# Optimization experiments

Hardware: AMD Instinct MI355X
Metric: run time of the kernel (lower is better)

## Reference

```python
import jax, jax.numpy as jnp
import numpy as np

T, B, NA = 32, 32, 5          # timesteps, envs, actions
HID, FEAT = 256, 512          # lstm hidden, cnn features
IN_DIM = FEAT + NA            # lstm input size (517)
FLAT = 64 * 7 * 7             # cnn flatten size (3136)


def _conv(x, w, b, s):
    # x: NCHW, w: OIHW, VALID padding, stride s
    y = jax.lax.conv_general_dilated(x, w, (s, s), 'VALID',
                                     dimension_numbers=('NCHW', 'OIHW', 'NCHW'))
    return y + b[None, :, None, None]


def setup_inputs() -> dict:
    key = jax.random.key(0)
    ks = jax.random.split(key, 24)
    p = lambda k, shape: (jax.random.normal(k, shape, jnp.float32) * 0.05)
    return {
        'image': jax.random.uniform(ks[0], (T * B, 3, 84, 84), jnp.float32) * 255.0,
        'last_action': jax.random.randint(ks[1], (T * B,), 0, NA),
        'done': jax.random.bernoulli(ks[2], 0.05, (T * B,)).astype(jnp.float32),
        'h0': jnp.zeros((B, HID), jnp.float32),
        'c0': jnp.zeros((B, HID), jnp.float32),
        # NatureCNN params
        'W1': p(ks[3], (32, 3, 8, 8)), 'b1': jnp.zeros((32,), jnp.float32),
        'W2': p(ks[4], (64, 32, 4, 4)), 'b2': jnp.zeros((64,), jnp.float32),
        'W3': p(ks[5], (64, 64, 3, 3)), 'b3': jnp.zeros((64,), jnp.float32),
        'Wfc': p(ks[6], (FEAT, FLAT)), 'bfc': jnp.zeros((FEAT,), jnp.float32),
        # LSTM params (torch gate order i,f,g,o)
        'W_ih': p(ks[7], (4 * HID, IN_DIM)), 'W_hh': p(ks[8], (4 * HID, HID)),
        'b_ih': jnp.zeros((4 * HID,), jnp.float32), 'b_hh': jnp.zeros((4 * HID,), jnp.float32),
        # policy MLP (hidden 64, tanh)
        'Wp1': p(ks[9], (64, HID)), 'bp1': jnp.zeros((64,), jnp.float32),
        'Wp2': p(ks[10], (NA, 64)) * 0.01, 'bp2': jnp.zeros((NA,), jnp.float32),
        # value MLP
        'Wv1': p(ks[11], (64, HID)), 'bv1': jnp.zeros((64,), jnp.float32),
        'Wv2': p(ks[12], (1, 64)), 'bv2': jnp.zeros((1,), jnp.float32),
    }


def reference(image, last_action, done, h0, c0,
              W1, b1, W2, b2, W3, b3, Wfc, bfc,
              W_ih, W_hh, b_ih, b_hh,
              Wp1, bp1, Wp2, bp2, Wv1, bv1, Wv2, bv2):
    # --- extract: NatureCNN + one-hot(last_action) ---
    x = image / 255.0
    x = jax.nn.relu(_conv(x, W1, b1, 4))   # (TB,32,20,20)
    x = jax.nn.relu(_conv(x, W2, b2, 2))   # (TB,64,9,9)
    x = jax.nn.relu(_conv(x, W3, b3, 1))   # (TB,64,7,7)
    x = x.reshape(x.shape[0], -1)
    feat = jax.nn.relu(x @ Wfc.T + bfc)    # (TB,512)
    oh = jax.nn.one_hot(last_action, NA, dtype=feat.dtype)
    xs = jnp.concatenate([feat, oh], axis=1).reshape(T, B, IN_DIM)
    ds = done.reshape(T, B)

    # --- remember: done-masked LSTM recurrence (torch gate order i,f,g,o) ---
    def step(carry, inp):
        h, c = carry
        xt, dt = inp
        m = (1.0 - dt)[:, None]
        h = h * m
        c = c * m
        g = xt @ W_ih.T + b_ih + h @ W_hh.T + b_hh   # (B, 4*HID)
        i, f, gg, o = jnp.split(g, 4, axis=1)
        c = jax.nn.sigmoid(f) * c + jax.nn.sigmoid(i) * jnp.tanh(gg)
        h = jax.nn.sigmoid(o) * jnp.tanh(c)
        return (h, c), h

    (hT, cT), hs = jax.lax.scan(step, (h0, c0), (xs, ds))
    h = hs.reshape(T * B, HID)

    # --- heads ---
    logits = jnp.tanh(h @ Wp1.T + bp1) @ Wp2.T + bp2   # (TB, NA)
    v = jnp.tanh(h @ Wv1.T + bv1) @ Wv2.T + bv2        # (TB, 1)
    return logits, v, hT, cT
```

## Files before the change

### kernel.cpp

```cpp
#include <hip/hip_runtime.h>
#include <math.h>

typedef float  f4v __attribute__((ext_vector_type(4)));
typedef short  s8v __attribute__((ext_vector_type(8)));
typedef int    i4v __attribute__((ext_vector_type(4)));

__device__ __forceinline__ float sigm(float x) { return 1.f / (1.f + expf(-x)); }
__device__ __forceinline__ unsigned short f2bf(float f) {
    unsigned int u = __float_as_uint(f);
    return (unsigned short)((u + 0x7FFF + ((u >> 16) & 1)) >> 16);
}
__device__ __forceinline__ s8v pack8(float4 a, float4 b) {
    union { unsigned short u[8]; s8v v; } r;
    r.u[0] = f2bf(a.x); r.u[1] = f2bf(a.y); r.u[2] = f2bf(a.z); r.u[3] = f2bf(a.w);
    r.u[4] = f2bf(b.x); r.u[5] = f2bf(b.y); r.u[6] = f2bf(b.z); r.u[7] = f2bf(b.w);
    return r.v;
}

__global__ __launch_bounds__(256) void k_amax(const float* __restrict__ Whh,
                                              unsigned int* __restrict__ amax_bits) {
    int i = blockIdx.x * 256 + threadIdx.x;
    float v = fabsf(Whh[i]);
#pragma unroll
    for (int o = 1; o < 64; o <<= 1) v = fmaxf(v, __shfl_xor(v, o));
    if ((threadIdx.x & 63) == 0) atomicMax(amax_bits, __float_as_uint(v));
}

__global__ __launch_bounds__(256) void k_prep(const float* __restrict__ W2, const float* __restrict__ W3,
                                              const float* __restrict__ Wfc, const float* __restrict__ Wih,
                                              const float* __restrict__ W1, const float* __restrict__ Whh,
                                              const unsigned int* __restrict__ amax_bits,
                                              unsigned short* __restrict__ W2p, unsigned short* __restrict__ W3p,
                                              unsigned short* __restrict__ Wfcp, unsigned short* __restrict__ Wihp,
                                              unsigned short* __restrict__ W1p, signed char* __restrict__ Wq) {
    int i = blockIdx.x * 256 + threadIdx.x;
    if (i < 32768) {
        W2p[i] = f2bf(W2[i]);
    } else if (i < 98304) {
        int j = i - 32768;
        int co = j >> 10, r = j & 1023, ci = r >> 4, s = r & 15, ky = s >> 2, kx = s & 3;
        W3p[j] = (ky < 3 && kx < 3) ? f2bf(W3[((co * 64 + ci) * 3 + ky) * 3 + kx]) : (unsigned short)0;
    } else if (i < 1703936) {
        int j = i - 98304;
        Wfcp[j] = f2bf(Wfc[j]);
    } else if (i < 2228224) {
        int j = i - 1703936;
        int n = j >> 9, k = j & 511;
        Wihp[j] = f2bf(Wih[n * 517 + k]);
    } else if (i < 2234368) {
        int j = i - 2228224;
        W1p[j] = f2bf(W1[j] * (1.f / 255.f));
    } else if (i < 2496512) {
        int j = i - 2234368;
        float amax = __uint_as_float(amax_bits[0]);
        float s = 127.f / amax;
        int qv = (int)rintf(Whh[j] * s);
        qv = qv > 127 ? 127 : (qv < -127 ? -127 : qv);
        Wq[j] = (signed char)qv;
    }
}

__global__ __launch_bounds__(256) void k_conv1(const float* __restrict__ img,
                                               const unsigned short* __restrict__ Bw,
                                               const float* __restrict__ bias,
                                               unsigned short* __restrict__ out) {
    __shared__ unsigned short c1s[32][260];
    int lane = threadIdx.x & 63, w = threadIdx.x >> 6;
    int l15 = lane & 15, q = lane >> 4;
    int m0 = blockIdx.x * 256;
    const float* Ap[4];
#pragma unroll
    for (int mf = 0; mf < 4; ++mf) {
        int m = m0 + w * 64 + mf * 16 + l15;
        int im = m / 400, p = m - im * 400;
        int oy = p / 20, ox = p - oy * 20;
        Ap[mf] = img + im * 21168 + oy * 336 + ox * 4;
    }
    const unsigned short* Bp0 = Bw + l15 * 192 + q * 8;
    const unsigned short* Bp1 = Bw + (16 + l15) * 192 + q * 8;
    s8v bf0[6], bf1[6];
#pragma unroll
    for (int ks = 0; ks < 6; ++ks) {
        bf0[ks] = *(const s8v*)(Bp0 + ks * 32);
        bf1[ks] = *(const s8v*)(Bp1 + ks * 32);
    }
    f4v acc[8];
#pragma unroll
    for (int i = 0; i < 8; ++i) acc[i] = (f4v){0.f, 0.f, 0.f, 0.f};
#pragma unroll
    for (int ks = 0; ks < 6; ++ks) {
        int k0 = ks * 32 + q * 8;
        int c = k0 >> 6, ky = (k0 >> 3) & 7;
        int roff = c * 7056 + ky * 84;
        s8v ua[4];
#pragma unroll
        for (int mf = 0; mf < 4; ++mf) {
            float4 a0 = *(const float4*)(Ap[mf] + roff);
            float4 a1 = *(const float4*)(Ap[mf] + roff + 4);
            ua[mf] = pack8(a0, a1);
        }
#pragma unroll
        for (int mf = 0; mf < 4; ++mf) {
            acc[mf * 2 + 0] = __builtin_amdgcn_mfma_f32_16x16x32_bf16(ua[mf], bf0[ks], acc[mf * 2 + 0], 0, 0, 0);
            acc[mf * 2 + 1] = __builtin_amdgcn_mfma_f32_16x16x32_bf16(ua[mf], bf1[ks], acc[mf * 2 + 1], 0, 0, 0);
        }
    }
#pragma unroll
    for (int nf = 0; nf < 2; ++nf) {
        int n = nf * 16 + l15;
        float b = bias[n];
#pragma unroll
        for (int mf = 0; mf < 4; ++mf) {
#pragma unroll
            for (int r = 0; r < 4; ++r) {
                int ml = w * 64 + mf * 16 + q * 4 + r;
                float v = acc[mf * 2 + nf][r] + b;
                c1s[n][ml] = f2bf(v > 0.f ? v : 0.f);
            }
        }
    }
    __syncthreads();
#pragma unroll
    for (int seg = 0; seg < 32; ++seg) {
        int flat = seg * 256 + threadIdx.x;
        int n = flat >> 8, ml = flat & 255;
        int m = m0 + ml;
        int im = m / 400, p = m - im * 400;
        out[(im * 32 + n) * 400 + p] = c1s[n][ml];
    }
}

__global__ __launch_bounds__(256) void k_conv2(const unsigned short* __restrict__ A,
                                               const unsigned short* __restrict__ Bw,
                                               const float* __restrict__ bias,
                                               unsigned short* __restrict__ out) {
    __shared__ unsigned short c2s[64][136];
    int lane = threadIdx.x & 63, w = threadIdx.x >> 6;
    int l15 = lane & 15, q = lane >> 4;
    int m0 = blockIdx.x * 128;
    int ma = m0 + w * 32 + l15, mb = ma + 16;
    int ia = ma / 81, pa = ma - ia * 81; int oya = pa / 9, oxa = pa - oya * 9;
    int ib = mb / 81, pb = mb - ib * 81; int oyb = pb / 9, oxb = pb - oyb * 9;
    const unsigned short* Aa = A + ia * 12800 + oya * 40 + oxa * 2 + (q & 1) * 40;
    const unsigned short* Ab = A + ib * 12800 + oyb * 40 + oxb * 2 + (q & 1) * 40;
    int ci0 = q >> 1;
    const unsigned short* B0 = Bw + (l15) * 512 + q * 8;
    const unsigned short* B1 = Bw + (16 + l15) * 512 + q * 8;
    const unsigned short* B2 = Bw + (32 + l15) * 512 + q * 8;
    const unsigned short* B3 = Bw + (48 + l15) * 512 + q * 8;
    f4v acc[8];
#pragma unroll
    for (int i = 0; i < 8; ++i) acc[i] = (f4v){0.f, 0.f, 0.f, 0.f};
    for (int c = 0; c < 16; ++c) {
        int ci = 2 * c + ci0;
        const unsigned short* pa_ = Aa + ci * 400;
        const unsigned short* pb_ = Ab + ci * 400;
        union { unsigned int u[4]; s8v v; } ua, ub;
        ua.u[0] = *(const unsigned int*)(pa_);      ua.u[1] = *(const unsigned int*)(pa_ + 2);
        ua.u[2] = *(const unsigned int*)(pa_ + 20); ua.u[3] = *(const unsigned int*)(pa_ + 22);
        ub.u[0] = *(const unsigned int*)(pb_);      ub.u[1] = *(const unsigned int*)(pb_ + 2);
        ub.u[2] = *(const unsigned int*)(pb_ + 20); ub.u[3] = *(const unsigned int*)(pb_ + 22);
        s8v b0 = *(const s8v*)B0, b1 = *(const s8v*)B1, b2 = *(const s8v*)B2, b3 = *(const s8v*)B3;
        B0 += 32; B1 += 32; B2 += 32; B3 += 32;
        acc[0] = __builtin_amdgcn_mfma_f32_16x16x32_bf16(ua.v, b0, acc[0], 0, 0, 0);
        acc[1] = __builtin_amdgcn_mfma_f32_16x16x32_bf16(ua.v, b1, acc[1], 0, 0, 0);
        acc[2] = __builtin_amdgcn_mfma_f32_16x16x32_bf16(ua.v, b2, acc[2], 0, 0, 0);
        acc[3] = __builtin_amdgcn_mfma_f32_16x16x32_bf16(ua.v, b3, acc[3], 0, 0, 0);
        acc[4] = __builtin_amdgcn_mfma_f32_16x16x32_bf16(ub.v, b0, acc[4], 0, 0, 0);
        acc[5] = __builtin_amdgcn_mfma_f32_16x16x32_bf16(ub.v, b1, acc[5], 0, 0, 0);
        acc[6] = __builtin_amdgcn_mfma_f32_16x16x32_bf16(ub.v, b2, acc[6], 0, 0, 0);
        acc[7] = __builtin_amdgcn_mfma_f32_16x16x32_bf16(ub.v, b3, acc[7], 0, 0, 0);
    }
#pragma unroll
    for (int nf = 0; nf < 4; ++nf) {
        int n = nf * 16 + l15;
        float b = bias[n];
#pragma unroll
        for (int mf = 0; mf < 2; ++mf) {
#pragma unroll
            for (int r = 0; r < 4; ++r) {
                int ml = w * 32 + mf * 16 + q * 4 + r;
                float v = acc[mf * 4 + nf][r] + b;
                c2s[n][ml] = f2bf(v > 0.f ? v : 0.f);
            }
        }
    }
    __syncthreads();
#pragma unroll
    for (int seg = 0; seg < 32; ++seg) {
        int flat = seg * 256 + threadIdx.x;
        int n = flat >> 7, ml = flat & 127;
        int m = m0 + ml;
        int im = m / 81, p = m - im * 81;
        out[im * 5184 + n * 81 + p] = c2s[n][ml];
    }
}

__global__ __launch_bounds__(256) void k_conv3(const unsigned short* __restrict__ A,
                                               const unsigned short* __restrict__ Bw,
                                               const float* __restrict__ bias,
                                               unsigned short* __restrict__ out) {
    __shared__ unsigned short c3s[64][136];
    int lane = threadIdx.x & 63, w = threadIdx.x >> 6;
    int l15 = lane & 15, q = lane >> 4;
    int m0 = blockIdx.x * 128;
    int ma = m0 + w * 32 + l15, mb = ma + 16;
    int ia = ma / 49, pa = ma - ia * 49; int oya = pa / 7, oxa = pa - oya * 7;
    int ib = mb / 49, pb = mb - ib * 49; int oyb = pb / 7, oxb = pb - oyb * 7;
    int ky0 = (q & 1) * 2;
    int r0off = ky0 * 9;
    int r1off = (ky0 + 1 > 2 ? 2 : ky0 + 1) * 9;
    int zr = q & 1;
    const unsigned short* Aa = A + ia * 5184 + oya * 9 + oxa;
    const unsigned short* Ab = A + ib * 5184 + oyb * 9 + oxb;
    int ci0 = q >> 1;
    const unsigned short* B0 = Bw + (l15) * 1024 + q * 8;
    const unsigned short* B1 = Bw + (16 + l15) * 1024 + q * 8;
    const unsigned short* B2 = Bw + (32 + l15) * 1024 + q * 8;
    const unsigned short* B3 = Bw + (48 + l15) * 1024 + q * 8;
    f4v acc[8];
#pragma unroll
    for (int i = 0; i < 8; ++i) acc[i] = (f4v){0.f, 0.f, 0.f, 0.f};
    for (int c = 0; c < 32; ++c) {
        int ci = 2 * c + ci0;
        const unsigned short* pa_ = Aa + ci * 81;
        const unsigned short* pb_ = Ab + ci * 81;
        s8v av, bv;
        av[0] = pa_[r0off]; av[1] = pa_[r0off + 1]; av[2] = pa_[r0off + 2]; av[3] = 0;
        av[4] = zr ? (short)0 : (short)pa_[r1off];
        av[5] = zr ? (short)0 : (short)pa_[r1off + 1];
        av[6] = zr ? (short)0 : (short)pa_[r1off + 2];
        av[7] = 0;
        bv[0] = pb_[r0off]; bv[1] = pb_[r0off + 1]; bv[2] = pb_[r0off + 2]; bv[3] = 0;
        bv[4] = zr ? (short)0 : (short)pb_[r1off];
        bv[5] = zr ? (short)0 : (short)pb_[r1off + 1];
        bv[6] = zr ? (short)0 : (short)pb_[r1off + 2];
        bv[7] = 0;
        s8v b0 = *(const s8v*)B0, b1 = *(const s8v*)B1, b2 = *(const s8v*)B2, b3 = *(const s8v*)B3;
        B0 += 32; B1 += 32; B2 += 32; B3 += 32;
        acc[0] = __builtin_amdgcn_mfma_f32_16x16x32_bf16(av, b0, acc[0], 0, 0, 0);
        acc[1] = __builtin_amdgcn_mfma_f32_16x16x32_bf16(av, b1, acc[1], 0, 0, 0);
        acc[2] = __builtin_amdgcn_mfma_f32_16x16x32_bf16(av, b2, acc[2], 0, 0, 0);
        acc[3] = __builtin_amdgcn_mfma_f32_16x16x32_bf16(av, b3, acc[3], 0, 0, 0);
        acc[4] = __builtin_amdgcn_mfma_f32_16x16x32_bf16(bv, b0, acc[4], 0, 0, 0);
        acc[5] = __builtin_amdgcn_mfma_f32_16x16x32_bf16(bv, b1, acc[5], 0, 0, 0);
        acc[6] = __builtin_amdgcn_mfma_f32_16x16x32_bf16(bv, b2, acc[6], 0, 0, 0);
        acc[7] = __builtin_amdgcn_mfma_f32_16x16x32_bf16(bv, b3, acc[7], 0, 0, 0);
    }
#pragma unroll
    for (int nf = 0; nf < 4; ++nf) {
        int n = nf * 16 + l15;
        float b = bias[n];
#pragma unroll
        for (int mf = 0; mf < 2; ++mf) {
#pragma unroll
            for (int r = 0; r < 4; ++r) {
                int ml = w * 32 + mf * 16 + q * 4 + r;
                float v = acc[mf * 4 + nf][r] + b;
                c3s[n][ml] = f2bf(v > 0.f ? v : 0.f);
            }
        }
    }
    __syncthreads();
#pragma unroll
    for (int seg = 0; seg < 32; ++seg) {
        int flat = seg * 256 + threadIdx.x;
        int n = flat >> 7, ml = flat & 127;
        int m = m0 + ml;
        int im = m / 49, p = m - im * 49;
        out[im * 3136 + n * 49 + p] = c3s[n][ml];
    }
}

__global__ __launch_bounds__(256) void k_fc(const unsigned short* __restrict__ A,
                                            const unsigned short* __restrict__ Bw,
                                            const float* __restrict__ bias,
                                            unsigned short* __restrict__ out) {
    int lane = threadIdx.x & 63, w = threadIdx.x >> 6;
    int l15 = lane & 15, q = lane >> 4;
    int m0 = blockIdx.x * 32 + (w & 1) * 16;
    int n0 = blockIdx.y * 64 + (w >> 1) * 32;
    const unsigned short* Ap = A + (m0 + l15) * 3136 + q * 8;
    const unsigned short* B0 = Bw + (n0 + l15) * 3136 + q * 8;
    const unsigned short* B1 = B0 + 16 * 3136;
    f4v acc0 = (f4v){0.f, 0.f, 0.f, 0.f}, acc1 = (f4v){0.f, 0.f, 0.f, 0.f};
    for (int c = 0; c < 98; ++c) {
        s8v av = *(const s8v*)Ap;
        s8v b0 = *(const s8v*)B0;
        s8v b1 = *(const s8v*)B1;
        Ap += 32; B0 += 32; B1 += 32;
        acc0 = __builtin_amdgcn_mfma_f32_16x16x32_bf16(av, b0, acc0, 0, 0, 0);
        acc1 = __builtin_amdgcn_mfma_f32_16x16x32_bf16(av, b1, acc1, 0, 0, 0);
    }
    float bi0 = bias[n0 + l15], bi1 = bias[n0 + 16 + l15];
#pragma unroll
    for (int r = 0; r < 4; ++r) {
        int m = m0 + q * 4 + r;
        float v0 = acc0[r] + bi0; v0 = v0 > 0.f ? v0 : 0.f;
        float v1 = acc1[r] + bi1; v1 = v1 > 0.f ? v1 : 0.f;
        out[m * 512 + n0 + l15] = f2bf(v0);
        out[m * 512 + n0 + 16 + l15] = f2bf(v1);
    }
}

__global__ __launch_bounds__(256) void k_gx(const unsigned short* __restrict__ A,
                                            const unsigned short* __restrict__ Bw,
                                            const float* __restrict__ Wih,
                                            const float* __restrict__ bih,
                                            const float* __restrict__ bhh,
                                            const int* __restrict__ act,
                                            float* __restrict__ out) {
    int lane = threadIdx.x & 63, w = threadIdx.x >> 6;
    int l15 = lane & 15, q = lane >> 4;
    int m0 = blockIdx.x * 32 + (w & 1) * 16;
    int n0 = blockIdx.y * 64 + (w >> 1) * 32;
    const unsigned short* Ap = A + (m0 + l15) * 512 + q * 8;
    const unsigned short* B0 = Bw + (n0 + l15) * 512 + q * 8;
    const unsigned short* B1 = B0 + 16 * 512;
    f4v acc0 = (f4v){0.f, 0.f, 0.f, 0.f}, acc1 = (f4v){0.f, 0.f, 0.f, 0.f};
    for (int c = 0; c < 16; ++c) {
        s8v av = *(const s8v*)Ap;
        s8v b0 = *(const s8v*)B0;
        s8v b1 = *(const s8v*)B1;
        Ap += 32; B0 += 32; B1 += 32;
        acc0 = __builtin_amdgcn_mfma_f32_16x16x32_bf16(av, b0, acc0, 0, 0, 0);
        acc1 = __builtin_amdgcn_mfma_f32_16x16x32_bf16(av, b1, acc1, 0, 0, 0);
    }
    int na = n0 + l15, nb = n0 + 16 + l15;
    float ca = bih[na] + bhh[na], cb_ = bih[nb] + bhh[nb];
#pragma unroll
    for (int r = 0; r < 4; ++r) {
        int m = m0 + q * 4 + r;
        int a = act[m];
        out[m * 1024 + na] = acc0[r] + Wih[na * 517 + 512 + a] + ca;
        out[m * 1024 + nb] = acc1[r] + Wih[nb * 517 + 512 + a] + cb_;
    }
}

__global__ __launch_bounds__(1024) void k_lstm_all(const float* __restrict__ h0,
                                                   const float* __restrict__ c0,
                                                   const float* __restrict__ done,
                                                   const float* __restrict__ gx,
                                                   const signed char* __restrict__ Wq,
                                                   const unsigned int* __restrict__ amax_bits,
                                                   float* __restrict__ hs,
                                                   float* __restrict__ cb) {
    int b = blockIdx.x;
    int tid = threadIdx.x;
    int w = tid >> 6, lane = tid & 63;
    int l15 = lane & 15, q = lane >> 4;
    __shared__ float gbuf[1024];
    __shared__ float cst[256];
    __shared__ signed char hA[4][64][16];

    i4v wfr[4][4];
    const signed char* wb = Wq + (w * 64 + l15) * 256 + q * 16;
#pragma unroll
    for (int s = 0; s < 4; ++s)
#pragma unroll
        for (int kf = 0; kf < 4; ++kf)
            wfr[s][kf] = *(const i4v*)(wb + s * 16 * 256 + kf * 64);
    float sw = __uint_as_float(amax_bits[0]) * (1.f / (127.f * 127.f));

    ((int*)hA)[tid] = 0;
    __syncthreads();
    if (tid < 256) {
        int u = tid;
        cst[u] = c0[b * 256 + u];
        float m0v = 1.f - done[b];
        float hv = h0[b * 256 + u] * m0v;
        hv = hv > 1.f ? 1.f : (hv < -1.f ? -1.f : hv);
        hA[u >> 6][((u >> 4) & 3) * 16][u & 15] = (signed char)(int)rintf(hv * 127.f);
    }
    __syncthreads();

    for (int t = 0; t < 32; ++t) {
        float gxi = 0.f, gxf = 0.f, gxg = 0.f, gxo = 0.f, dcur = 0.f, dnxt = 0.f;
        if (tid < 256) {
            const float* gr = gx + (t * 32 + b) * 1024;
            gxi = gr[tid]; gxf = gr[256 + tid]; gxg = gr[512 + tid]; gxo = gr[768 + tid];
            dcur = done[t * 32 + b];
            dnxt = (t < 31) ? done[(t + 1) * 32 + b] : 1.f;
        }
        i4v acc[4];
#pragma unroll
        for (int s = 0; s < 4; ++s) acc[s] = (i4v){0, 0, 0, 0};
#pragma unroll
        for (int kf = 0; kf < 4; ++kf) {
            i4v a = *(const i4v*)&hA[kf][lane][0];
#pragma unroll
            for (int s = 0; s < 4; ++s)
                acc[s] = __builtin_amdgcn_mfma_i32_16x16x64_i8(a, wfr[s][kf], acc[s], 0, 0, 0);
        }
        if (q == 0) {
#pragma unroll
            for (int s = 0; s < 4; ++s)
                gbuf[w * 64 + s * 16 + l15] = (float)acc[s][0];
        }
        __syncthreads();
        if (tid < 256) {
            int u = tid;
            float gi = gbuf[u] * sw + gxi;
            float gf = gbuf[256 + u] * sw + gxf;
            float gg = gbuf[512 + u] * sw + gxg;
            float go = gbuf[768 + u] * sw + gxo;
            float cm = cst[u] * (1.f - dcur);
            float cn = sigm(gf) * cm + sigm(gi) * tanhf(gg);
            float hn = sigm(go) * tanhf(cn);
            cst[u] = cn;
            hs[t * 8192 + b * 256 + u] = hn;
            float hv = hn * (1.f - dnxt);
            hA[u >> 6][((u >> 4) & 3) * 16][u & 15] = (signed char)(int)rintf(hv * 127.f);
        }
        __syncthreads();
    }
    if (tid < 256) cb[b * 256 + tid] = cst[tid];
}

__global__ __launch_bounds__(256) void k_heads(const float* __restrict__ hs,
                                               const float* __restrict__ cb,
                                               const float* __restrict__ Wp1, const float* __restrict__ bp1,
                                               const float* __restrict__ Wp2, const float* __restrict__ bp2,
                                               const float* __restrict__ Wv1, const float* __restrict__ bv1,
                                               const float* __restrict__ Wv2, const float* __restrict__ bv2,
                                               float* __restrict__ out) {
    int lane = threadIdx.x & 63;
    int m = blockIdx.x * 4 + (threadIdx.x >> 6);
    const float4* hv = (const float4*)(hs + m * 256);
    const float4* wp = (const float4*)(Wp1 + lane * 256);
    const float4* wq = (const float4*)(Wv1 + lane * 256);
    float ap = 0.f, av = 0.f;
#pragma unroll 8
    for (int k = 0; k < 64; ++k) {
        float4 h4 = hv[k];
        float4 p4 = wp[k];
        float4 q4 = wq[k];
        ap += h4.x * p4.x + h4.y * p4.y + h4.z * p4.z + h4.w * p4.w;
        av += h4.x * q4.x + h4.y * q4.y + h4.z * q4.z + h4.w * q4.w;
    }
    float hp = tanhf(ap + bp1[lane]);
    float hq = tanhf(av + bv1[lane]);
#pragma unroll
    for (int j = 0; j < 5; ++j) {
        float s = hp * Wp2[j * 64 + lane];
        s += __shfl_xor(s, 1); s += __shfl_xor(s, 2); s += __shfl_xor(s, 4);
        s += __shfl_xor(s, 8); s += __shfl_xor(s, 16); s += __shfl_xor(s, 32);
        if (lane == 0) out[m * 5 + j] = s + bp2[j];
    }
    float s = hq * Wv2[lane];
    s += __shfl_xor(s, 1); s += __shfl_xor(s, 2); s += __shfl_xor(s, 4);
    s += __shfl_xor(s, 8); s += __shfl_xor(s, 16); s += __shfl_xor(s, 32);
    if (lane == 0) out[5120 + m] = s + bv2[0];

    int g = blockIdx.x * 256 + threadIdx.x;
    if (g < 8192) {
        out[6144 + g] = hs[31 * 8192 + g];
        out[6144 + 8192 + g] = cb[g];
    }
}

extern "C" void kernel_launch(void* const* d_in, const int* in_sizes, int n_in,
                              void* d_out, int out_size, void* d_ws, size_t ws_size,
                              hipStream_t stream) {
    const float* image = (const float*)d_in[0];
    const int*   act   = (const int*)d_in[1];
    const float* done  = (const float*)d_in[2];
    const float* h0    = (const float*)d_in[3];
    const float* c0    = (const float*)d_in[4];
    const float* W1    = (const float*)d_in[5];
    const float* b1    = (const float*)d_in[6];
    const float* W2    = (const float*)d_in[7];
    const float* b2    = (const float*)d_in[8];
    const float* W3    = (const float*)d_in[9];
    const float* b3    = (const float*)d_in[10];
    const float* Wfc   = (const float*)d_in[11];
    const float* bfc   = (const float*)d_in[12];
    const float* Wih   = (const float*)d_in[13];
    const float* Whh   = (const float*)d_in[14];
    const float* bih   = (const float*)d_in[15];
    const float* bhh   = (const float*)d_in[16];
    const float* Wp1   = (const float*)d_in[17];
    const float* bp1   = (const float*)d_in[18];
    const float* Wp2   = (const float*)d_in[19];
    const float* bp2   = (const float*)d_in[20];
    const float* Wv1   = (const float*)d_in[21];
    const float* bv1   = (const float*)d_in[22];
    const float* Wv2   = (const float*)d_in[23];
    const float* bv2   = (const float*)d_in[24];
    float* out = (float*)d_out;
    char* base = (char*)d_ws;

    unsigned short* a1   = (unsigned short*)(base);
    unsigned short* a2   = (unsigned short*)(base + 26214432);
    unsigned short* W2p  = (unsigned short*)(base + 36831328);
    unsigned short* W3p  = W2p + 32768;
    unsigned short* Wfcp = W2p + 98304;
    unsigned short* Wihp = W2p + 1703936;
    unsigned short* W1p  = (unsigned short*)(base + 41287776);
    unsigned int*   amax = (unsigned int*)(base + 41300064);
    signed char*    Wq   = (signed char*)(base + 41300096);
    unsigned short* a3   = (unsigned short*)(base);
    unsigned short* feat = (unsigned short*)(base + 6422528);
    float* gx = (float*)(base + 7471104);
    float* hs = (float*)(base + 11665408);
    float* cb = (float*)(base + 12713984);

    hipMemsetAsync(amax, 0, 4, stream);
    k_amax<<<1024, 256, 0, stream>>>(Whh, amax);
    k_prep<<<9752, 256, 0, stream>>>(W2, W3, Wfc, Wih, W1, Whh, amax, W2p, W3p, Wfcp, Wihp, W1p, Wq);
    k_conv1<<<1600, 256, 0, stream>>>(image, W1p, b1, a1);
    k_conv2<<<648, 256, 0, stream>>>(a1, W2p, b2, a2);
    k_conv3<<<392, 256, 0, stream>>>(a2, W3p, b3, a3);
    k_fc<<<dim3(32, 8), 256, 0, stream>>>(a3, Wfcp, bfc, feat);
    k_gx<<<dim3(32, 16), 256, 0, stream>>>(feat, Wihp, Wih, bih, bhh, act, gx);
    k_lstm_all<<<32, 1024, 0, stream>>>(h0, c0, done, gx, Wq, amax, hs, cb);
    k_heads<<<256, 256, 0, stream>>>(hs, cb, Wp1, bp1, Wp2, bp2, Wv1, bv1, Wv2, bv2, out);
}
```

Before: 453.1 us.

## Software-prefetch operands in conv/fc loops and use packed bf16 conversion

Adds register double-buffering to the conv1, conv2, conv3 and fc main loops, so the next iteration's A and B operands are loaded before the current MFMAs are issued. This is meant to hide global memory latency behind matrix math. It also replaces the manual round-to-nearest bf16 conversion with the hardware v_cvt_pk_bf16_f32 instruction, which converts two floats at once. The epilogues now write two bf16 values per 32-bit LDS store. The risks are higher register pressure and possible rounding differences from the hardware conversion.

```diff
diff --git a/kernel.cpp b/kernel.cpp
--- a/kernel.cpp
+++ b/kernel.cpp
@@ -10,10 +10,15 @@
     unsigned int u = __float_as_uint(f);
     return (unsigned short)((u + 0x7FFF + ((u >> 16) & 1)) >> 16);
 }
+__device__ __forceinline__ unsigned int cvt2(float lo, float hi) {
+    unsigned int r;
+    asm("v_cvt_pk_bf16_f32 %0, %1, %2" : "=v"(r) : "v"(lo), "v"(hi));
+    return r;
+}
 __device__ __forceinline__ s8v pack8(float4 a, float4 b) {
-    union { unsigned short u[8]; s8v v; } r;
-    r.u[0] = f2bf(a.x); r.u[1] = f2bf(a.y); r.u[2] = f2bf(a.z); r.u[3] = f2bf(a.w);
-    r.u[4] = f2bf(b.x); r.u[5] = f2bf(b.y); r.u[6] = f2bf(b.z); r.u[7] = f2bf(b.w);
+    union { unsigned int u[4]; s8v v; } r;
+    r.u[0] = cvt2(a.x, a.y); r.u[1] = cvt2(a.z, a.w);
+    r.u[2] = cvt2(b.x, b.y); r.u[3] = cvt2(b.z, b.w);
     return r.v;
 }
 
@@ -84,25 +89,41 @@
         bf0[ks] = *(const s8v*)(Bp0 + ks * 32);
         bf1[ks] = *(const s8v*)(Bp1 + ks * 32);
     }
-    f4v acc[8];
-#pragma unroll
-    for (int i = 0; i < 8; ++i) acc[i] = (f4v){0.f, 0.f, 0.f, 0.f};
+    int roffs[6];
 #pragma unroll
     for (int ks = 0; ks < 6; ++ks) {
         int k0 = ks * 32 + q * 8;
         int c = k0 >> 6, ky = (k0 >> 3) & 7;
-        int roff = c * 7056 + ky * 84;
-        s8v ua[4];
+        roffs[ks] = c * 7056 + ky * 84;
+    }
+    f4v acc[8];
+#pragma unroll
+    for (int i = 0; i < 8; ++i) acc[i] = (f4v){0.f, 0.f, 0.f, 0.f};
+    float4 ca[4], cb[4];
+#pragma unroll
+    for (int mf = 0; mf < 4; ++mf) {
+        ca[mf] = *(const float4*)(Ap[mf] + roffs[0]);
+        cb[mf] = *(const float4*)(Ap[mf] + roffs[0] + 4);
+    }
+#pragma unroll
+    for (int ks = 0; ks < 6; ++ks) {
+        float4 na[4], nb[4];
+        if (ks < 5) {
+#pragma unroll
+            for (int mf = 0; mf < 4; ++mf) {
+                na[mf] = *(const float4*)(Ap[mf] + roffs[ks + 1]);
+                nb[mf] = *(const float4*)(Ap[mf] + roffs[ks + 1] + 4);
+            }
+        }
 #pragma unroll
         for (int mf = 0; mf < 4; ++mf) {
-            float4 a0 = *(const float4*)(Ap[mf] + roff);
-            float4 a1 = *(const float4*)(Ap[mf] + roff + 4);
-            ua[mf] = pack8(a0, a1);
-        }
-#pragma unroll
-        for (int mf = 0; mf < 4; ++mf) {
-            acc[mf * 2 + 0] = __builtin_amdgcn_mfma_f32_16x16x32_bf16(ua[mf], bf0[ks], acc[mf * 2 + 0], 0, 0, 0);
-            acc[mf * 2 + 1] = __builtin_amdgcn_mfma_f32_16x16x32_bf16(ua[mf], bf1[ks], acc[mf * 2 + 1], 0, 0, 0);
+            s8v ua = pack8(ca[mf], cb[mf]);
+            acc[mf * 2 + 0] = __builtin_amdgcn_mfma_f32_16x16x32_bf16(ua, bf0[ks], acc[mf * 2 + 0], 0, 0, 0);
+            acc[mf * 2 + 1] = __builtin_amdgcn_mfma_f32_16x16x32_bf16(ua, bf1[ks], acc[mf * 2 + 1], 0, 0, 0);
+        }
+        if (ks < 5) {
+#pragma unroll
+            for (int mf = 0; mf < 4; ++mf) { ca[mf] = na[mf]; cb[mf] = nb[mf]; }
         }
     }
 #pragma unroll
@@ -111,11 +132,12 @@
         float b = bias[n];
 #pragma unroll
         for (int mf = 0; mf < 4; ++mf) {
-#pragma unroll
-            for (int r = 0; r < 4; ++r) {
-                int ml = w * 64 + mf * 16 + q * 4 + r;
-                float v = acc[mf * 2 + nf][r] + b;
-                c1s[n][ml] = f2bf(v > 0.f ? v : 0.f);
+            int ml = w * 64 + mf * 16 + q * 4;
+#pragma unroll
+            for (int r = 0; r < 4; r += 2) {
+                float v0 = acc[mf * 2 + nf][r] + b;     v0 = v0 > 0.f ? v0 : 0.f;
+                float v1 = acc[mf * 2 + nf][r + 1] + b; v1 = v1 > 0.f ? v1 : 0.f;
+                *(unsigned int*)&c1s[n][ml + r] = cvt2(v0, v1);
             }
         }
     }
@@ -151,17 +173,25 @@
     f4v acc[8];
 #pragma unroll
     for (int i = 0; i < 8; ++i) acc[i] = (f4v){0.f, 0.f, 0.f, 0.f};
+    union AU { unsigned int u[4]; s8v v; };
+    const unsigned short* pa_ = Aa + ci0 * 400;
+    const unsigned short* pb_ = Ab + ci0 * 400;
+    AU ua, ub;
+    ua.u[0] = *(const unsigned int*)(pa_);      ua.u[1] = *(const unsigned int*)(pa_ + 2);
+    ua.u[2] = *(const unsigned int*)(pa_ + 20); ua.u[3] = *(const unsigned int*)(pa_ + 22);
+    ub.u[0] = *(const unsigned int*)(pb_);      ub.u[1] = *(const unsigned int*)(pb_ + 2);
+    ub.u[2] = *(const unsigned int*)(pb_ + 20); ub.u[3] = *(const unsigned int*)(pb_ + 22);
+    s8v b0 = *(const s8v*)B0, b1 = *(const s8v*)B1, b2 = *(const s8v*)B2, b3 = *(const s8v*)B3;
     for (int c = 0; c < 16; ++c) {
-        int ci = 2 * c + ci0;
-        const unsigned short* pa_ = Aa + ci * 400;
-        const unsigned short* pb_ = Ab + ci * 400;
-        union { unsigned int u[4]; s8v v; } ua, ub;
-        ua.u[0] = *(const unsigned int*)(pa_);      ua.u[1] = *(const unsigned int*)(pa_ + 2);
-        ua.u[2] = *(const unsigned int*)(pa_ + 20); ua.u[3] = *(const unsigned int*)(pa_ + 22);
-        ub.u[0] = *(const unsigned int*)(pb_);      ub.u[1] = *(const unsigned int*)(pb_ + 2);
-        ub.u[2] = *(const unsigned int*)(pb_ + 20); ub.u[3] = *(const unsigned int*)(pb_ + 22);
-        s8v b0 = *(const s8v*)B0, b1 = *(const s8v*)B1, b2 = *(const s8v*)B2, b3 = *(const s8v*)B3;
-        B0 += 32; B1 += 32; B2 += 32; B3 += 32;
+        AU nua, nub; s8v nb0, nb1, nb2, nb3;
+        if (c < 15) {
+            pa_ += 800; pb_ += 800; B0 += 32; B1 += 32; B2 += 32; B3 += 32;
+            nua.u[0] = *(const unsigned int*)(pa_);      nua.u[1] = *(const unsigned int*)(pa_ + 2);
+            nua.u[2] = *(const unsigned int*)(pa_ + 20); nua.u[3] = *(const unsigned int*)(pa_ + 22);
+            nub.u[0] = *(const unsigned int*)(pb_);      nub.u[1] = *(const unsigned int*)(pb_ + 2);
+            nub.u[2] = *(const unsigned int*)(pb_ + 20); nub.u[3] = *(const unsigned int*)(pb_ + 22);
+            nb0 = *(const s8v*)B0; nb1 = *(const s8v*)B1; nb2 = *(const s8v*)B2; nb3 = *(const s8v*)B3;
+        }
         acc[0] = __builtin_amdgcn_mfma_f32_16x16x32_bf16(ua.v, b0, acc[0], 0, 0, 0);
         acc[1] = __builtin_amdgcn_mfma_f32_16x16x32_bf16(ua.v, b1, acc[1], 0, 0, 0);
         acc[2] = __builtin_amdgcn_mfma_f32_16x16x32_bf16(ua.v, b2, acc[2], 0, 0, 0);
@@ -170,6 +200,7 @@
         acc[5] = __builtin_amdgcn_mfma_f32_16x16x32_bf16(ub.v, b1, acc[5], 0, 0, 0);
         acc[6] = __builtin_amdgcn_mfma_f32_16x16x32_bf16(ub.v, b2, acc[6], 0, 0, 0);
         acc[7] = __builtin_amdgcn_mfma_f32_16x16x32_bf16(ub.v, b3, acc[7], 0, 0, 0);
+        if (c < 15) { ua = nua; ub = nub; b0 = nb0; b1 = nb1; b2 = nb2; b3 = nb3; }
     }
 #pragma unroll
     for (int nf = 0; nf < 4; ++nf) {
@@ -177,11 +208,12 @@
         float b = bias[n];
 #pragma unroll
         for (int mf = 0; mf < 2; ++mf) {
-#pragma unroll
-            for (int r = 0; r < 4; ++r) {
-                int ml = w * 32 + mf * 16 + q * 4 + r;
-                float v = acc[mf * 4 + nf][r] + b;
-                c2s[n][ml] = f2bf(v > 0.f ? v : 0.f);
+            int ml = w * 32 + mf * 16 + q * 4;
+#pragma unroll
+            for (int r = 0; r < 4; r += 2) {
+                float v0 = acc[mf * 4 + nf][r] + b;     v0 = v0 > 0.f ? v0 : 0.f;
+                float v1 = acc[mf * 4 + nf][r + 1] + b; v1 = v1 > 0.f ? v1 : 0.f;
+                *(unsigned int*)&c2s[n][ml + r] = cvt2(v0, v1);
             }
         }
     }
@@ -221,23 +253,35 @@
     f4v acc[8];
 #pragma unroll
     for (int i = 0; i < 8; ++i) acc[i] = (f4v){0.f, 0.f, 0.f, 0.f};
+    const unsigned short* pa_ = Aa + ci0 * 81;
+    const unsigned short* pb_ = Ab + ci0 * 81;
+    unsigned short ca_[6], cb_[6];
+    ca_[0] = pa_[r0off]; ca_[1] = pa_[r0off + 1]; ca_[2] = pa_[r0off + 2];
+    ca_[3] = pa_[r1off]; ca_[4] = pa_[r1off + 1]; ca_[5] = pa_[r1off + 2];
+    cb_[0] = pb_[r0off]; cb_[1] = pb_[r0off + 1]; cb_[2] = pb_[r0off + 2];
+    cb_[3] = pb_[r1off]; cb_[4] = pb_[r1off + 1]; cb_[5] = pb_[r1off + 2];
+    s8v b0 = *(const s8v*)B0, b1 = *(const s8v*)B1, b2 = *(const s8v*)B2, b3 = *(const s8v*)B3;
     for (int c = 0; c < 32; ++c) {
-        int ci = 2 * c + ci0;
-        const unsigned short* pa_ = Aa + ci * 81;
-        const unsigned short* pb_ = Ab + ci * 81;
+        unsigned short na_[6], nb_[6]; s8v nb0, nb1, nb2, nb3;
+        if (c < 31) {
+            pa_ += 162; pb_ += 162; B0 += 32; B1 += 32; B2 += 32; B3 += 32;
+            na_[0] = pa_[r0off]; na_[1] = pa_[r0off + 1]; na_[2] = pa_[r0off + 2];
+            na_[3] = pa_[r1off]; na_[4] = pa_[r1off + 1]; na_[5] = pa_[r1off + 2];
+            nb_[0] = pb_[r0off]; nb_[1] = pb_[r0off + 1]; nb_[2] = pb_[r0off + 2];
+            nb_[3] = pb_[r1off]; nb_[4] = pb_[r1off + 1]; nb_[5] = pb_[r1off + 2];
+            nb0 = *(const s8v*)B0; nb1 = *(const s8v*)B1; nb2 = *(const s8v*)B2; nb3 = *(const s8v*)B3;
+        }
         s8v av, bv;
-        av[0] = pa_[r0off]; av[1] = pa_[r0off + 1]; av[2] = pa_[r0off + 2]; av[3] = 0;
-        av[4] = zr ? (short)0 : (short)pa_[r1off];
-        av[5] = zr ? (short)0 : (short)pa_[r1off + 1];
-        av[6] = zr ? (short)0 : (short)pa_[r1off + 2];
+        av[0] = (short)ca_[0]; av[1] = (short)ca_[1]; av[2] = (short)ca_[2]; av[3] = 0;
+        av[4] = zr ? (short)0 : (short)ca_[3];
+        av[5] = zr ? (short)0 : (short)ca_[4];
+        av[6] = zr ? (short)0 : (short)ca_[5];
         av[7] = 0;
-        bv[0] = pb_[r0off]; bv[1] = pb_[r0off + 1]; bv[2] = pb_[r0off + 2]; bv[3] = 0;
-        bv[4] = zr ? (short)0 : (short)pb_[r1off];
-        bv[5] = zr ? (short)0 : (short)pb_[r1off + 1];
-        bv[6] = zr ? (short)0 : (short)pb_[r1off + 2];
+        bv[0] = (short)cb_[0]; bv[1] = (short)cb_[1]; bv[2] = (short)cb_[2]; bv[3] = 0;
+        bv[4] = zr ? (short)0 : (short)cb_[3];
+        bv[5] = zr ? (short)0 : (short)cb_[4];
+        bv[6] = zr ? (short)0 : (short)cb_[5];
         bv[7] = 0;
-        s8v b0 = *(const s8v*)B0, b1 = *(const s8v*)B1, b2 = *(const s8v*)B2, b3 = *(const s8v*)B3;
-        B0 += 32; B1 += 32; B2 += 32; B3 += 32;
         acc[0] = __builtin_amdgcn_mfma_f32_16x16x32_bf16(av, b0, acc[0], 0, 0, 0);
         acc[1] = __builtin_amdgcn_mfma_f32_16x16x32_bf16(av, b1, acc[1], 0, 0, 0);
         acc[2] = __builtin_amdgcn_mfma_f32_16x16x32_bf16(av, b2, acc[2], 0, 0, 0);
@@ -246,6 +290,11 @@
         acc[5] = __builtin_amdgcn_mfma_f32_16x16x32_bf16(bv, b1, acc[5], 0, 0, 0);
         acc[6] = __builtin_amdgcn_mfma_f32_16x16x32_bf16(bv, b2, acc[6], 0, 0, 0);
         acc[7] = __builtin_amdgcn_mfma_f32_16x16x32_bf16(bv, b3, acc[7], 0, 0, 0);
+        if (c < 31) {
+#pragma unroll
+            for (int j = 0; j < 6; ++j) { ca_[j] = na_[j]; cb_[j] = nb_[j]; }
+            b0 = nb0; b1 = nb1; b2 = nb2; b3 = nb3;
+        }
     }
 #pragma unroll
     for (int nf = 0; nf < 4; ++nf) {
@@ -253,11 +302,12 @@
         float b = bias[n];
 #pragma unroll
         for (int mf = 0; mf < 2; ++mf) {
-#pragma unroll
-            for (int r = 0; r < 4; ++r) {
-                int ml = w * 32 + mf * 16 + q * 4 + r;
-                float v = acc[mf * 4 + nf][r] + b;
-                c3s[n][ml] = f2bf(v > 0.f ? v : 0.f);
+            int ml = w * 32 + mf * 16 + q * 4;
+#pragma unroll
+            for (int r = 0; r < 4; r += 2) {
+                float v0 = acc[mf * 4 + nf][r] + b;     v0 = v0 > 0.f ? v0 : 0.f;
+                float v1 = acc[mf * 4 + nf][r + 1] + b; v1 = v1 > 0.f ? v1 : 0.f;
+                *(unsigned int*)&c3s[n][ml + r] = cvt2(v0, v1);
             }
         }
     }
@@ -284,14 +334,16 @@
     const unsigned short* B0 = Bw + (n0 + l15) * 3136 + q * 8;
     const unsigned short* B1 = B0 + 16 * 3136;
     f4v acc0 = (f4v){0.f, 0.f, 0.f, 0.f}, acc1 = (f4v){0.f, 0.f, 0.f, 0.f};
-    for (int c = 0; c < 98; ++c) {
-        s8v av = *(const s8v*)Ap;
-        s8v b0 = *(const s8v*)B0;
-        s8v b1 = *(const s8v*)B1;
+    s8v av = *(const s8v*)Ap, b0 = *(const s8v*)B0, b1 = *(const s8v*)B1;
+    for (int c = 0; c < 97; ++c) {
         Ap += 32; B0 += 32; B1 += 32;
+        s8v nav = *(const s8v*)Ap, nb0 = *(const s8v*)B0, nb1 = *(const s8v*)B1;
         acc0 = __builtin_amdgcn_mfma_f32_16x16x32_bf16(av, b0, acc0, 0, 0, 0);
         acc1 = __builtin_amdgcn_mfma_f32_16x16x32_bf16(av, b1, acc1, 0, 0, 0);
-    }
+        av = nav; b0 = nb0; b1 = nb1;
+    }
+    acc0 = __builtin_amdgcn_mfma_f32_16x16x32_bf16(av, b0, acc0, 0, 0, 0);
+    acc1 = __builtin_amdgcn_mfma_f32_16x16x32_bf16(av, b1, acc1, 0, 0, 0);
     float bi0 = bias[n0 + l15], bi1 = bias[n0 + 16 + l15];
 #pragma unroll
     for (int r = 0; r < 4; ++r) {
```

Result: no change. 452.2 us (-0.2%).
